# Performance work log

Measured on AMD Instinct MI355X. Metric: run time of the kernel, lower is better.

## Reference

```python
import jax, jax.numpy as jnp
import numpy as np

DEPTH, DIM, HEADS, HD, CTX, B = 4, 768, 12, 64, 2048, 4
INNER = HEADS * HD  # 768
EPS = 1e-5  # torch LayerNorm default


def _ln(x, g, b):
    m = jnp.mean(x, axis=-1, keepdims=True)
    v = jnp.var(x, axis=-1, keepdims=True)
    return (x - m) * jax.lax.rsqrt(v + EPS) * g + b


def setup_inputs() -> dict:
    key = jax.random.key(0)
    ks = jax.random.split(key, 12)
    s = 0.02
    return {
        "x": jax.random.normal(ks[0], (B, CTX, DIM), dtype=jnp.float32),
        "pos_emb": jax.random.normal(ks[1], (1, CTX, DIM), dtype=jnp.float32),
        # per-layer params stacked on leading depth axis
        "ln1_g": jnp.ones((DEPTH, DIM), jnp.float32),
        "ln1_b": jnp.zeros((DEPTH, DIM), jnp.float32),
        "Wq": jax.random.normal(ks[2], (DEPTH, DIM, INNER), dtype=jnp.float32) * s,
        "Wk": jax.random.normal(ks[3], (DEPTH, DIM, INNER), dtype=jnp.float32) * s,
        "Wv": jax.random.normal(ks[4], (DEPTH, DIM, INNER), dtype=jnp.float32) * s,
        "Wo": jax.random.normal(ks[5], (DEPTH, INNER, DIM), dtype=jnp.float32) * s,
        "ln2_g": jnp.ones((DEPTH, DIM), jnp.float32),
        "ln2_b": jnp.zeros((DEPTH, DIM), jnp.float32),
        "W1": jax.random.normal(ks[6], (DEPTH, DIM, DIM), dtype=jnp.float32) * s,  # hidden_dim == dim per source
        "b1": jnp.zeros((DEPTH, DIM), jnp.float32),
        "W2": jax.random.normal(ks[7], (DEPTH, DIM, DIM), dtype=jnp.float32) * s,
        "b2": jnp.zeros((DEPTH, DIM), jnp.float32),
    }


def reference(x, pos_emb, ln1_g, ln1_b, Wq, Wk, Wv, Wo, ln2_g, ln2_b, W1, b1, W2, b2):
    scale = 1.0 / np.sqrt(HD).astype(np.float32)
    x = x + pos_emb
    b, n, _ = x.shape
    for i in range(DEPTH):
        # --- attention block (pre-LN, residual) ---
        h = _ln(x, ln1_g[i], ln1_b[i])
        q = (h @ Wq[i]).reshape(b, n, HEADS, HD)
        k = (h @ Wk[i]).reshape(b, n, HEADS, HD)
        v = (h @ Wv[i]).reshape(b, n, HEADS, HD)
        scores = jnp.einsum('bihd,bjhd->bhij', q, k) * scale
        attn = jax.nn.softmax(scores, axis=-1)
        o = jnp.einsum('bhij,bjhd->bihd', attn, v).reshape(b, n, INNER)
        x = x + o @ Wo[i]
        # --- feed-forward block (LN -> Linear -> GELU -> Linear, residual) ---
        h = _ln(x, ln2_g[i], ln2_b[i])
        h = jax.nn.gelu(h @ W1[i] + b1[i], approximate=False)
        x = x + (h @ W2[i] + b2[i])
    return x
```

## Files before the change

### kernel.cpp

```cpp
#include <hip/hip_runtime.h>
#include <math.h>


#define DEPTH 4
#define DIM   768
#define HEADS 12
#define HD    64
#define CTXN  2048
#define BATCH 4
#define TOKENS (BATCH * CTXN)
#define QKVS  (3 * DIM)

typedef unsigned short u16;
typedef short s16x8 __attribute__((ext_vector_type(8)));
typedef float f32x4 __attribute__((ext_vector_type(4)));
typedef u16  u16x4 __attribute__((ext_vector_type(4)));

__device__ __forceinline__ u16 f2bf(float f) {
  union { float f; unsigned u; } c;
  c.f = f;
  unsigned u = c.u;
  return (u16)((u + 0x7FFFu + ((u >> 16) & 1u)) >> 16);
}

__device__ __forceinline__ s16x8 ldfrag(const u16* t, int r, int g) {
  return *(const s16x8*)(t + r * 64 + 8 * (g ^ (r & 7)));
}
__device__ __forceinline__ void stfrag(u16* t, int r, int g, s16x8 v) {
  *(s16x8*)(t + r * 64 + 8 * (g ^ (r & 7))) = v;
}

__device__ __forceinline__ void gld_lds16(const u16* g, u16* l) {
#if __has_builtin(__builtin_amdgcn_global_load_lds)
  __builtin_amdgcn_global_load_lds(
      (const __attribute__((address_space(1))) unsigned int*)g,
      (__attribute__((address_space(3))) unsigned int*)l, 16, 0, 0);
#else
  int lane = threadIdx.x & 63;
  *(s16x8*)(l + lane * 8) = *(const s16x8*)(g);
#endif
}

__global__ __launch_bounds__(256) void add_pos_kernel(
    const float* __restrict__ X, const float* __restrict__ P,
    float* __restrict__ Y, int n, int pn) {
  int i = blockIdx.x * 256 + threadIdx.x;
  if (i < n) Y[i] = X[i] + P[i % pn];
}

__global__ __launch_bounds__(256) void wconv_kernel(
    const float* __restrict__ Wq, const float* __restrict__ Wk,
    const float* __restrict__ Wv, const float* __restrict__ Wo,
    const float* __restrict__ W1, const float* __restrict__ W2,
    u16* __restrict__ dst) {
  int mat = blockIdx.z;
  int layer = mat / 6, type = mat % 6;
  const float* srcs[6] = {Wq, Wk, Wv, Wo, W1, W2};
  const float* src = srcs[type] + (size_t)layer * DIM * DIM;
  u16* d = dst + (size_t)mat * DIM * DIM;
  __shared__ float L[32][33];
  int k0 = blockIdx.y * 32, n0 = blockIdx.x * 32;
  int r = threadIdx.x >> 3, c4 = (threadIdx.x & 7) * 4;
  float4 v = *(const float4*)&src[(size_t)(k0 + r) * DIM + n0 + c4];
  L[c4 + 0][r] = v.x; L[c4 + 1][r] = v.y;
  L[c4 + 2][r] = v.z; L[c4 + 3][r] = v.w;
  __syncthreads();
  u16x4 w;
#pragma unroll
  for (int j = 0; j < 4; ++j) w[j] = f2bf(L[r][c4 + j]);
  *(u16x4*)&d[(size_t)(n0 + r) * DIM + k0 + c4] = w;
}

__global__ __launch_bounds__(256) void ln_kernel(
    const float* __restrict__ X, const float* __restrict__ g,
    const float* __restrict__ b, u16* __restrict__ Y) {
  int t = blockIdx.x;
  int tid = threadIdx.x;
  const float* xr = X + (size_t)t * DIM;
  float v0 = xr[tid], v1 = xr[tid + 256], v2 = xr[tid + 512];
  float s = v0 + v1 + v2;
  float q = v0 * v0 + v1 * v1 + v2 * v2;
#pragma unroll
  for (int o = 32; o > 0; o >>= 1) {
    s += __shfl_xor(s, o);
    q += __shfl_xor(q, o);
  }
  __shared__ float rs[4], rq[4];
  int w = tid >> 6;
  if ((tid & 63) == 0) { rs[w] = s; rq[w] = q; }
  __syncthreads();
  s = rs[0] + rs[1] + rs[2] + rs[3];
  q = rq[0] + rq[1] + rq[2] + rq[3];
  float mean = s * (1.0f / DIM);
  float var  = q * (1.0f / DIM) - mean * mean;
  float r = rsqrtf(var + 1e-5f);
  u16* yr = Y + (size_t)t * DIM;
  yr[tid]       = f2bf((v0 - mean) * r * g[tid]       + b[tid]);
  yr[tid + 256] = f2bf((v1 - mean) * r * g[tid + 256] + b[tid + 256]);
  yr[tid + 512] = f2bf((v2 - mean) * r * g[tid + 512] + b[tid + 512]);
}

template <int HAS_BIAS, int HAS_GELU, int HAS_RES, int OUT_BF16>
__global__ __launch_bounds__(256, 3) void gemm_bf16(
    const u16* __restrict__ A, const u16* __restrict__ Bt,
    const float* __restrict__ bias, void* __restrict__ Cv, int Nc) {
  float* C = (float*)Cv;
  u16* Cb = (u16*)Cv;
  __shared__ __align__(16) u16 As[128 * 64];
  __shared__ __align__(16) u16 Bs[128 * 64];
  int tid = threadIdx.x;
  int wave = tid >> 6, lane = tid & 63, ln = lane & 15, quad = lane >> 4;
  int wr = wave >> 1, wc = wave & 1;
  int m0 = blockIdx.y * 128, n0 = blockIdx.x * 128;

  int srow = wave * 32 + (lane >> 3);
  int sg = (lane & 7) ^ ((lane >> 3) & 7);
  const u16* ga = A + (size_t)(m0 + srow) * DIM + sg * 8;
  const u16* gb = Bt + (size_t)(n0 + srow) * DIM + sg * 8;
  u16* la = As + wave * 2048;
  u16* lb = Bs + wave * 2048;

  f32x4 acc[4][4];
  const f32x4 zero = {0.0f, 0.0f, 0.0f, 0.0f};
#pragma unroll
  for (int i = 0; i < 4; ++i)
#pragma unroll
    for (int j = 0; j < 4; ++j) acc[i][j] = zero;

  for (int kt = 0; kt < DIM / 64; ++kt) {
#pragma unroll
    for (int i = 0; i < 4; ++i) {
      gld_lds16(ga + (size_t)i * 8 * DIM, la + i * 512);
      gld_lds16(gb + (size_t)i * 8 * DIM, lb + i * 512);
    }
    ga += 64; gb += 64;
    __syncthreads();

    s16x8 bfr0[4], bfr1[4];
#pragma unroll
    for (int ni = 0; ni < 4; ++ni) {
      bfr0[ni] = ldfrag(Bs, wc * 64 + ni * 16 + ln, quad);
      bfr1[ni] = ldfrag(Bs, wc * 64 + ni * 16 + ln, 4 + quad);
    }
#pragma unroll
    for (int mi = 0; mi < 4; ++mi) {
      s16x8 a0 = ldfrag(As, wr * 64 + mi * 16 + ln, quad);
      s16x8 a1 = ldfrag(As, wr * 64 + mi * 16 + ln, 4 + quad);
#pragma unroll
      for (int ni = 0; ni < 4; ++ni) {
        acc[mi][ni] = __builtin_amdgcn_mfma_f32_16x16x32_bf16(a0, bfr0[ni], acc[mi][ni], 0, 0, 0);
        acc[mi][ni] = __builtin_amdgcn_mfma_f32_16x16x32_bf16(a1, bfr1[ni], acc[mi][ni], 0, 0, 0);
      }
    }
    __syncthreads();
  }

#pragma unroll
  for (int ni = 0; ni < 4; ++ni) {
    int c = n0 + wc * 64 + ni * 16 + ln;
    float bv = HAS_BIAS ? bias[c] : 0.0f;
#pragma unroll
    for (int mi = 0; mi < 4; ++mi) {
#pragma unroll
      for (int reg = 0; reg < 4; ++reg) {
        int r = m0 + wr * 64 + mi * 16 + quad * 4 + reg;
        float v = acc[mi][ni][reg] + bv;
        if (HAS_GELU) v = 0.5f * v * (1.0f + erff(v * 0.70710678118654752f));
        size_t o = (size_t)r * Nc + c;
        if (OUT_BF16) { Cb[o] = f2bf(v); }
        else if (HAS_RES) { C[o] += v; }
        else { C[o] = v; }
      }
    }
  }
}

__global__ __launch_bounds__(256) void vtrans_kernel(
    const u16* __restrict__ QKV, u16* __restrict__ Vt) {
  int bid = blockIdx.x;
  int tt = bid & 31;
  int h  = (bid >> 5) % HEADS;
  int b  = bid / (32 * HEADS);
  int tid = threadIdx.x;
  __shared__ u16 T[64][66];
  const u16* src = QKV + ((size_t)(b * CTXN + tt * 64)) * QKVS + 2 * DIM + h * HD;
#pragma unroll
  for (int i = 0; i < 2; ++i) {
    int idx = tid + i * 256, r = idx >> 3, g = idx & 7;
    s16x8 v = *(const s16x8*)&src[(size_t)r * QKVS + g * 8];
#pragma unroll
    for (int j = 0; j < 8; ++j) T[g * 8 + j][r] = (u16)v[j];
  }
  __syncthreads();
#pragma unroll
  for (int i = 0; i < 2; ++i) {
    int idx = tid + i * 256, d = idx >> 3, g = idx & 7;
    s16x8 w;
#pragma unroll
    for (int j = 0; j < 8; ++j) w[j] = (short)T[d][g * 8 + j];
    *(s16x8*)&Vt[((size_t)(b * HEADS + h) * HD + d) * CTXN + tt * 64 + g * 8] = w;
  }
}

__global__ __launch_bounds__(256) void attn_kernel(
    const u16* __restrict__ QKV, const u16* __restrict__ Vt,
    u16* __restrict__ Ob) {
  const int tiles = CTXN / 64;
  int bid = blockIdx.x;
  int qt = bid % tiles;
  int h  = (bid / tiles) % HEADS;
  int b  = bid / (tiles * HEADS);
  int tid = threadIdx.x;
  int wave = tid >> 6, lane = tid & 63, ln = lane & 15, quad = lane >> 4;

  __shared__ __align__(16) char smem[24576];
  u16* Ks = (u16*)smem;
  u16* Vs = (u16*)(smem + 8192);
  u16* Ps = (u16*)(smem + 16384);
  float (*Of)[65] = (float (*)[65])smem;

  const u16* qrow =
      QKV + ((size_t)(b * CTXN + qt * 64 + wave * 16 + ln)) * QKVS + h * HD;
  s16x8 aq0 = *(const s16x8*)&qrow[quad * 8];
  s16x8 aq1 = *(const s16x8*)&qrow[32 + quad * 8];

  float m = -1e30f, l = 0.0f;
  f32x4 oacc[4];
  const f32x4 zero = {0.0f, 0.0f, 0.0f, 0.0f};
#pragma unroll
  for (int i = 0; i < 4; ++i) oacc[i] = zero;

  const u16* kb0 = QKV + ((size_t)b * CTXN) * QKVS + DIM + h * HD;
  const u16* vt0 = Vt + ((size_t)(b * HEADS + h) * HD) * CTXN;
  const float lg = 0.125f * 1.4426950408889634f;

  for (int kt = 0; kt < tiles; ++kt) {
#pragma unroll
    for (int i = 0; i < 2; ++i) {
      int idx = tid + i * 256, r = idx >> 3, g = idx & 7;
      stfrag(Ks, r, g, *(const s16x8*)&kb0[(size_t)(kt * 64 + r) * QKVS + g * 8]);
      stfrag(Vs, r, g, *(const s16x8*)&vt0[(size_t)r * CTXN + kt * 64 + g * 8]);
    }
    __syncthreads();

    f32x4 sacc[4];
#pragma unroll
    for (int nb = 0; nb < 4; ++nb) {
      sacc[nb] = zero;
      s16x8 k0 = ldfrag(Ks, nb * 16 + ln, quad);
      s16x8 k1 = ldfrag(Ks, nb * 16 + ln, 4 + quad);
      sacc[nb] = __builtin_amdgcn_mfma_f32_16x16x32_bf16(k0, aq0, sacc[nb], 0, 0, 0);
      sacc[nb] = __builtin_amdgcn_mfma_f32_16x16x32_bf16(k1, aq1, sacc[nb], 0, 0, 0);
    }

    float s2[4][4];
    float mx = -1e30f;
#pragma unroll
    for (int nb = 0; nb < 4; ++nb)
#pragma unroll
      for (int reg = 0; reg < 4; ++reg) {
        s2[nb][reg] = sacc[nb][reg] * lg;
        mx = fmaxf(mx, s2[nb][reg]);
      }
    mx = fmaxf(mx, __shfl_xor(mx, 16));
    mx = fmaxf(mx, __shfl_xor(mx, 32));
    float mnew = fmaxf(m, mx);
    float alpha = exp2f(m - mnew);
    float ls = 0.0f;
    u16x4 pk[4];
#pragma unroll
    for (int nb = 0; nb < 4; ++nb)
#pragma unroll
      for (int reg = 0; reg < 4; ++reg) {
        float p = exp2f(s2[nb][reg] - mnew);
        ls += p;
        pk[nb][reg] = f2bf(p);
      }
    ls += __shfl_xor(ls, 16);
    ls += __shfl_xor(ls, 32);
    l = l * alpha + ls;
    m = mnew;

    {
      int row = wave * 16 + ln;
      int rs = row & 7;
      int half = (quad & 1) * 4;
#pragma unroll
      for (int nb = 0; nb < 4; ++nb) {
        int g0 = nb * 2 + (quad >> 1);
        *(u16x4*)&Ps[row * 64 + 8 * (g0 ^ rs) + half] = pk[nb];
      }
    }
    __syncthreads();

    float ar[4];
#pragma unroll
    for (int reg = 0; reg < 4; ++reg) ar[reg] = __shfl(alpha, quad * 4 + reg);
#pragma unroll
    for (int nb = 0; nb < 4; ++nb)
#pragma unroll
      for (int reg = 0; reg < 4; ++reg) oacc[nb][reg] *= ar[reg];

    s16x8 ap0 = ldfrag(Ps, wave * 16 + ln, quad);
    s16x8 ap1 = ldfrag(Ps, wave * 16 + ln, 4 + quad);
#pragma unroll
    for (int nb = 0; nb < 4; ++nb) {
      s16x8 bv0 = ldfrag(Vs, nb * 16 + ln, quad);
      s16x8 bv1 = ldfrag(Vs, nb * 16 + ln, 4 + quad);
      oacc[nb] = __builtin_amdgcn_mfma_f32_16x16x32_bf16(ap0, bv0, oacc[nb], 0, 0, 0);
      oacc[nb] = __builtin_amdgcn_mfma_f32_16x16x32_bf16(ap1, bv1, oacc[nb], 0, 0, 0);
    }
    __syncthreads();
  }

  float li[4];
#pragma unroll
  for (int reg = 0; reg < 4; ++reg) li[reg] = 1.0f / __shfl(l, quad * 4 + reg);

#pragma unroll
  for (int nb = 0; nb < 4; ++nb)
#pragma unroll
    for (int reg = 0; reg < 4; ++reg)
      Of[wave * 16 + quad * 4 + reg][nb * 16 + ln] = oacc[nb][reg] * li[reg];
  __syncthreads();
  {
    int r = tid >> 2, c0 = (tid & 3) * 16;
    u16* dst = Ob + ((size_t)(b * CTXN + qt * 64 + r)) * DIM + h * HD + c0;
#pragma unroll
    for (int k = 0; k < 4; ++k) {
      u16x4 w;
#pragma unroll
      for (int j = 0; j < 4; ++j) w[j] = f2bf(Of[r][c0 + 4 * k + j]);
      *(u16x4*)&dst[4 * k] = w;
    }
  }
}

extern "C" void kernel_launch(void* const* d_in, const int* in_sizes, int n_in,
                              void* d_out, int out_size, void* d_ws, size_t ws_size,
                              hipStream_t stream) {
  const float* x_in  = (const float*)d_in[0];
  const float* pos   = (const float*)d_in[1];
  const float* ln1_g = (const float*)d_in[2];
  const float* ln1_b = (const float*)d_in[3];
  const float* Wq    = (const float*)d_in[4];
  const float* Wk    = (const float*)d_in[5];
  const float* Wv    = (const float*)d_in[6];
  const float* Wo    = (const float*)d_in[7];
  const float* ln2_g = (const float*)d_in[8];
  const float* ln2_b = (const float*)d_in[9];
  const float* W1    = (const float*)d_in[10];
  const float* b1    = (const float*)d_in[11];
  const float* W2    = (const float*)d_in[12];
  const float* b2    = (const float*)d_in[13];

  float* x = (float*)d_out;
  const size_t TD = (size_t)TOKENS * DIM;
  u16* hb  = (u16*)d_ws;
  u16* qkv = hb + TD;
  u16* vt  = qkv + 3 * TD;
  u16* wt  = vt + TD;
  u16* fb  = qkv;

  int n = (int)TD, pn = CTXN * DIM;
  add_pos_kernel<<<(n + 255) / 256, 256, 0, stream>>>(x_in, pos, x, n, pn);
  {
    dim3 wg(24, 24, 24);
    wconv_kernel<<<wg, 256, 0, stream>>>(Wq, Wk, Wv, Wo, W1, W2, wt);
  }

  const size_t WSZ = (size_t)DIM * DIM;
  dim3 gq(QKVS / 128, TOKENS / 128);
  dim3 gg(DIM / 128, TOKENS / 128);
  int nblk_attn = BATCH * HEADS * (CTXN / 64);
  for (int i = 0; i < DEPTH; ++i) {
    const u16* wqkv = wt + (size_t)(i * 6 + 0) * WSZ;
    const u16* wo   = wt + (size_t)(i * 6 + 3) * WSZ;
    const u16* w1   = wt + (size_t)(i * 6 + 4) * WSZ;
    const u16* w2   = wt + (size_t)(i * 6 + 5) * WSZ;

    ln_kernel<<<TOKENS, 256, 0, stream>>>(x, ln1_g + i * DIM, ln1_b + i * DIM, hb);
    gemm_bf16<0,0,0,1><<<gq, 256, 0, stream>>>(hb, wqkv, nullptr, qkv, QKVS);
    vtrans_kernel<<<nblk_attn, 256, 0, stream>>>(qkv, vt);
    attn_kernel<<<nblk_attn, 256, 0, stream>>>(qkv, vt, hb);
    gemm_bf16<0,0,1,0><<<gg, 256, 0, stream>>>(hb, wo, nullptr, x, DIM);

    ln_kernel<<<TOKENS, 256, 0, stream>>>(x, ln2_g + i * DIM, ln2_b + i * DIM, hb);
    gemm_bf16<1,1,0,1><<<gg, 256, 0, stream>>>(hb, w1, b1 + i * DIM, fb, DIM);
    gemm_bf16<1,0,1,0><<<gg, 256, 0, stream>>>(fb, w2, b2 + i * DIM, x, DIM);
  }
}
```

Before: 1.222 ms.

## Use hardware bf16 pack conversion and lazy softmax rescaling in attention

Replaces the software round-to-nearest bf16 conversion with the v_cvt_pk_bf16_f32 instruction in layernorm, GEMM epilogues and the attention output. In the attention inner loop, the running max is kept in unscaled units and the output and denominator are rescaled only when some lane's new max exceeds the old one by a threshold (a wave-wide vote). The scale and max subtraction are fused into a single fma. This removes per-tile rescale work and conversion ALU ops, at the cost of letting exponentials grow up to about 2^8 before renormalising and a divergent branch.

```diff
diff --git a/kernel.cpp b/kernel.cpp
--- a/kernel.cpp
+++ b/kernel.cpp
@@ -21,6 +21,15 @@
   c.f = f;
   unsigned u = c.u;
   return (u16)((u + 0x7FFFu + ((u >> 16) & 1u)) >> 16);
+}
+
+__device__ __forceinline__ unsigned cvt_pk_bf16(float lo, float hi) {
+  unsigned r;
+  asm("v_cvt_pk_bf16_f32 %0, %1, %2" : "=v"(r) : "v"(lo), "v"(hi));
+  return r;
+}
+__device__ __forceinline__ u16 bf1(float f) {
+  return (u16)cvt_pk_bf16(f, f);
 }
 
 __device__ __forceinline__ s16x8 ldfrag(const u16* t, int r, int g) {
@@ -95,9 +104,9 @@
   float var  = q * (1.0f / DIM) - mean * mean;
   float r = rsqrtf(var + 1e-5f);
   u16* yr = Y + (size_t)t * DIM;
-  yr[tid]       = f2bf((v0 - mean) * r * g[tid]       + b[tid]);
-  yr[tid + 256] = f2bf((v1 - mean) * r * g[tid + 256] + b[tid + 256]);
-  yr[tid + 512] = f2bf((v2 - mean) * r * g[tid + 512] + b[tid + 512]);
+  yr[tid]       = bf1((v0 - mean) * r * g[tid]       + b[tid]);
+  yr[tid + 256] = bf1((v1 - mean) * r * g[tid + 256] + b[tid + 256]);
+  yr[tid + 512] = bf1((v2 - mean) * r * g[tid + 512] + b[tid + 512]);
 }
 
 template <int HAS_BIAS, int HAS_GELU, int HAS_RES, int OUT_BF16>
@@ -167,7 +176,7 @@
         float v = acc[mi][ni][reg] + bv;
         if (HAS_GELU) v = 0.5f * v * (1.0f + erff(v * 0.70710678118654752f));
         size_t o = (size_t)r * Nc + c;
-        if (OUT_BF16) { Cb[o] = f2bf(v); }
+        if (OUT_BF16) { Cb[o] = bf1(v); }
         else if (HAS_RES) { C[o] += v; }
         else { C[o] = v; }
       }
@@ -233,6 +242,7 @@
   const u16* kb0 = QKV + ((size_t)b * CTXN) * QKVS + DIM + h * HD;
   const u16* vt0 = Vt + ((size_t)(b * HEADS + h) * HD) * CTXN;
   const float lg = 0.125f * 1.4426950408889634f;
+  const float THR = 44.3614195f;
 
   for (int kt = 0; kt < tiles; ++kt) {
 #pragma unroll
@@ -253,33 +263,44 @@
       sacc[nb] = __builtin_amdgcn_mfma_f32_16x16x32_bf16(k1, aq1, sacc[nb], 0, 0, 0);
     }
 
-    float s2[4][4];
-    float mx = -1e30f;
-#pragma unroll
-    for (int nb = 0; nb < 4; ++nb)
-#pragma unroll
-      for (int reg = 0; reg < 4; ++reg) {
-        s2[nb][reg] = sacc[nb][reg] * lg;
-        mx = fmaxf(mx, s2[nb][reg]);
-      }
+    float mx = fmaxf(fmaxf(sacc[0][0], sacc[0][1]), fmaxf(sacc[0][2], sacc[0][3]));
+#pragma unroll
+    for (int nb = 1; nb < 4; ++nb)
+      mx = fmaxf(mx, fmaxf(fmaxf(sacc[nb][0], sacc[nb][1]),
+                           fmaxf(sacc[nb][2], sacc[nb][3])));
     mx = fmaxf(mx, __shfl_xor(mx, 16));
     mx = fmaxf(mx, __shfl_xor(mx, 32));
-    float mnew = fmaxf(m, mx);
-    float alpha = exp2f(m - mnew);
+
+    if (!__all(mx <= m + THR)) {
+      float mnew = fmaxf(m, mx);
+      float alpha = exp2f((m - mnew) * lg);
+      float ar[4];
+#pragma unroll
+      for (int reg = 0; reg < 4; ++reg) ar[reg] = __shfl(alpha, quad * 4 + reg);
+#pragma unroll
+      for (int nb = 0; nb < 4; ++nb)
+#pragma unroll
+        for (int reg = 0; reg < 4; ++reg) oacc[nb][reg] *= ar[reg];
+      l *= alpha;
+      m = mnew;
+    }
+
+    float nm = -m * lg;
     float ls = 0.0f;
-    u16x4 pk[4];
-#pragma unroll
-    for (int nb = 0; nb < 4; ++nb)
-#pragma unroll
-      for (int reg = 0; reg < 4; ++reg) {
-        float p = exp2f(s2[nb][reg] - mnew);
-        ls += p;
-        pk[nb][reg] = f2bf(p);
-      }
+    uint2 pk[4];
+#pragma unroll
+    for (int nb = 0; nb < 4; ++nb) {
+      float p0 = exp2f(fmaf(sacc[nb][0], lg, nm));
+      float p1 = exp2f(fmaf(sacc[nb][1], lg, nm));
+      float p2 = exp2f(fmaf(sacc[nb][2], lg, nm));
+      float p3 = exp2f(fmaf(sacc[nb][3], lg, nm));
+      ls += (p0 + p1) + (p2 + p3);
+      pk[nb].x = cvt_pk_bf16(p0, p1);
+      pk[nb].y = cvt_pk_bf16(p2, p3);
+    }
     ls += __shfl_xor(ls, 16);
     ls += __shfl_xor(ls, 32);
-    l = l * alpha + ls;
-    m = mnew;
+    l += ls;
 
     {
       int row = wave * 16 + ln;
@@ -288,18 +309,10 @@
 #pragma unroll
       for (int nb = 0; nb < 4; ++nb) {
         int g0 = nb * 2 + (quad >> 1);
-        *(u16x4*)&Ps[row * 64 + 8 * (g0 ^ rs) + half] = pk[nb];
+        *(uint2*)&Ps[row * 64 + 8 * (g0 ^ rs) + half] = pk[nb];
       }
     }
     __syncthreads();
-
-    float ar[4];
-#pragma unroll
-    for (int reg = 0; reg < 4; ++reg) ar[reg] = __shfl(alpha, quad * 4 + reg);
-#pragma unroll
-    for (int nb = 0; nb < 4; ++nb)
-#pragma unroll
-      for (int reg = 0; reg < 4; ++reg) oacc[nb][reg] *= ar[reg];
 
     s16x8 ap0 = ldfrag(Ps, wave * 16 + ln, quad);
     s16x8 ap1 = ldfrag(Ps, wave * 16 + ln, 4 + quad);
@@ -328,10 +341,10 @@
     u16* dst = Ob + ((size_t)(b * CTXN + qt * 64 + r)) * DIM + h * HD + c0;
 #pragma unroll
     for (int k = 0; k < 4; ++k) {
-      u16x4 w;
-#pragma unroll
-      for (int j = 0; j < 4; ++j) w[j] = f2bf(Of[r][c0 + 4 * k + j]);
-      *(u16x4*)&dst[4 * k] = w;
+      uint2 w;
+      w.x = cvt_pk_bf16(Of[r][c0 + 4 * k + 0], Of[r][c0 + 4 * k + 1]);
+      w.y = cvt_pk_bf16(Of[r][c0 + 4 * k + 2], Of[r][c0 + 4 * k + 3]);
+      *(uint2*)&dst[4 * k] = w;
     }
   }
 }
```

After: 1.349 ms. 10.4% more time.

## Prefetch next K/V tile into registers and use lazy softmax rescaling in attention

Applied to the files above, without the earlier changes.

The attention loop now loads the next K/V tile into registers during compute of the current tile, overlapping global load latency with MFMA work. The online softmax skips the output rescale when the new row max stays within a threshold of the running max (checked wave-wide with __all), and folds the scale into an fma feeding exp2. This cuts per-tile rescale multiplies and shuffles. In exchange it uses more registers and bounds the exponent growth through the threshold.

```diff
diff --git a/kernel.cpp b/kernel.cpp
--- a/kernel.cpp
+++ b/kernel.cpp
@@ -233,15 +233,34 @@
   const u16* kb0 = QKV + ((size_t)b * CTXN) * QKVS + DIM + h * HD;
   const u16* vt0 = Vt + ((size_t)(b * HEADS + h) * HD) * CTXN;
   const float lg = 0.125f * 1.4426950408889634f;
+  const float THR = 44.3614195f;
+
+  int sr0 = tid >> 3, sg0 = tid & 7;
+  int sr1 = sr0 + 32;
+  const u16* kp0 = kb0 + (size_t)sr0 * QKVS + sg0 * 8;
+  const u16* kp1 = kb0 + (size_t)sr1 * QKVS + sg0 * 8;
+  const u16* vp0 = vt0 + (size_t)sr0 * CTXN + sg0 * 8;
+  const u16* vp1 = vt0 + (size_t)sr1 * CTXN + sg0 * 8;
+
+  s16x8 rk0 = *(const s16x8*)kp0;
+  s16x8 rk1 = *(const s16x8*)kp1;
+  s16x8 rv0 = *(const s16x8*)vp0;
+  s16x8 rv1 = *(const s16x8*)vp1;
 
   for (int kt = 0; kt < tiles; ++kt) {
-#pragma unroll
-    for (int i = 0; i < 2; ++i) {
-      int idx = tid + i * 256, r = idx >> 3, g = idx & 7;
-      stfrag(Ks, r, g, *(const s16x8*)&kb0[(size_t)(kt * 64 + r) * QKVS + g * 8]);
-      stfrag(Vs, r, g, *(const s16x8*)&vt0[(size_t)r * CTXN + kt * 64 + g * 8]);
-    }
+    stfrag(Ks, sr0, sg0, rk0);
+    stfrag(Ks, sr1, sg0, rk1);
+    stfrag(Vs, sr0, sg0, rv0);
+    stfrag(Vs, sr1, sg0, rv1);
     __syncthreads();
+
+    {
+      int ktn = (kt + 1 < tiles) ? kt + 1 : kt;
+      rk0 = *(const s16x8*)(kp0 + (size_t)ktn * 64 * QKVS);
+      rk1 = *(const s16x8*)(kp1 + (size_t)ktn * 64 * QKVS);
+      rv0 = *(const s16x8*)(vp0 + (size_t)ktn * 64);
+      rv1 = *(const s16x8*)(vp1 + (size_t)ktn * 64);
+    }
 
     f32x4 sacc[4];
 #pragma unroll
@@ -253,33 +272,43 @@
       sacc[nb] = __builtin_amdgcn_mfma_f32_16x16x32_bf16(k1, aq1, sacc[nb], 0, 0, 0);
     }
 
-    float s2[4][4];
-    float mx = -1e30f;
-#pragma unroll
-    for (int nb = 0; nb < 4; ++nb)
-#pragma unroll
-      for (int reg = 0; reg < 4; ++reg) {
-        s2[nb][reg] = sacc[nb][reg] * lg;
-        mx = fmaxf(mx, s2[nb][reg]);
-      }
+    float mx = fmaxf(fmaxf(sacc[0][0], sacc[0][1]), fmaxf(sacc[0][2], sacc[0][3]));
+#pragma unroll
+    for (int nb = 1; nb < 4; ++nb)
+      mx = fmaxf(mx, fmaxf(fmaxf(sacc[nb][0], sacc[nb][1]),
+                           fmaxf(sacc[nb][2], sacc[nb][3])));
     mx = fmaxf(mx, __shfl_xor(mx, 16));
     mx = fmaxf(mx, __shfl_xor(mx, 32));
-    float mnew = fmaxf(m, mx);
-    float alpha = exp2f(m - mnew);
+
+    if (!__all(mx <= m + THR)) {
+      float mnew = fmaxf(m, mx);
+      float alpha = exp2f((m - mnew) * lg);
+      float ar[4];
+#pragma unroll
+      for (int reg = 0; reg < 4; ++reg) ar[reg] = __shfl(alpha, quad * 4 + reg);
+#pragma unroll
+      for (int nb = 0; nb < 4; ++nb)
+#pragma unroll
+        for (int reg = 0; reg < 4; ++reg) oacc[nb][reg] *= ar[reg];
+      l *= alpha;
+      m = mnew;
+    }
+
+    float nm = -m * lg;
     float ls = 0.0f;
     u16x4 pk[4];
 #pragma unroll
-    for (int nb = 0; nb < 4; ++nb)
+    for (int nb = 0; nb < 4; ++nb) {
 #pragma unroll
       for (int reg = 0; reg < 4; ++reg) {
-        float p = exp2f(s2[nb][reg] - mnew);
+        float p = exp2f(fmaf(sacc[nb][reg], lg, nm));
         ls += p;
         pk[nb][reg] = f2bf(p);
       }
+    }
     ls += __shfl_xor(ls, 16);
     ls += __shfl_xor(ls, 32);
-    l = l * alpha + ls;
-    m = mnew;
+    l += ls;
 
     {
       int row = wave * 16 + ln;
@@ -292,14 +321,6 @@
       }
     }
     __syncthreads();
-
-    float ar[4];
-#pragma unroll
-    for (int reg = 0; reg < 4; ++reg) ar[reg] = __shfl(alpha, quad * 4 + reg);
-#pragma unroll
-    for (int nb = 0; nb < 4; ++nb)
-#pragma unroll
-      for (int reg = 0; reg < 4; ++reg) oacc[nb][reg] *= ar[reg];
 
     s16x8 ap0 = ldfrag(Ps, wave * 16 + ln, quad);
     s16x8 ap1 = ldfrag(Ps, wave * 16 + ln, 4 + quad);
```

After: 1.228 ms. Within noise of the previous version (+0.5%).
